# Kernel optimization log

Measured on AMD Instinct MI355X. Metric: run time of the kernel, lower is better.

## Reference

```python
import jax, jax.numpy as jnp
import numpy as np


def setup_inputs() -> dict:
    key = jax.random.key(0)
    k1, k2, k3, k4 = jax.random.split(key, 4)
    B, N, d_in, d_out = 8, 2048, 256, 256
    x = jax.random.normal(k1, (B, N, d_in), dtype=jnp.float32)
    adj_hat = jax.random.uniform(k2, (B, N, N), dtype=jnp.float32)
    W = jax.random.normal(k3, (d_out, d_in), dtype=jnp.float32) * (1.0 / np.sqrt(d_in))
    b = jax.random.normal(k4, (d_out,), dtype=jnp.float32) * 0.01
    return {"x": x, "adj_hat": adj_hat, "W": W, "b": b}


def reference(x, adj_hat, W, b):
    # Degrees from adj = adj_hat - I (i.e. without self loops): row sum minus diagonal.
    N = adj_hat.shape[1]
    diag = jnp.diagonal(adj_hat, axis1=-2, axis2=-1)          # [B, N]
    d = adj_hat.sum(axis=-1) - diag                           # [B, N]
    d_inv_sqrt = jnp.power(d, -0.5)                           # [B, N]
    # dad = D^-1/2 @ adj_hat @ D^-1/2  ==  d_i * a_ij * d_j (elementwise broadcast)
    dad = d_inv_sqrt[:, :, None] * adj_hat * d_inv_sqrt[:, None, :]  # [B, N, N]
    h = jnp.einsum('bnd,od->bno', x, W) + b                   # projection [B, N, d_out]
    return jnp.einsum('bnm,bmo->bno', dad, h)                 # [B, N, d_out]
```

## Files before the change

### kernel.cpp

```cpp
#include <hip/hip_runtime.h>
#include <hip/hip_bf16.h>


#define BATCH 8
#define NN    2048
#define DIN   256
#define DOUT  256
#define RTOT  (BATCH * NN)
#define AP    (NN + 32)
#define HP    (RTOT + 32)

typedef short  bf16x8  __attribute__((ext_vector_type(8)));
typedef short  short4v __attribute__((ext_vector_type(4)));
typedef float  f32x4   __attribute__((ext_vector_type(4)));

__device__ __forceinline__ short f2bf(float f) {
    union { float f; unsigned u; } v; v.f = f;
    unsigned r = v.u + 0x7fffu + ((v.u >> 16) & 1u);
    return (short)(r >> 16);
}

__device__ __forceinline__ void gl_lds16(const unsigned short* g, unsigned short* l) {
    __builtin_amdgcn_global_load_lds(
        (const __attribute__((address_space(1))) unsigned int*)g,
        (__attribute__((address_space(3))) unsigned int*)l, 16, 0, 0);
}

__global__ __launch_bounds__(256) void k_degree_cvt(const float* __restrict__ adj,
                                                    float* __restrict__ dis,
                                                    unsigned short* __restrict__ abf) {
    const int row = blockIdx.x;
    const int n = row & (NN - 1);
    const int tid = threadIdx.x;
    const float4* rp4 = (const float4*)(adj + (size_t)row * NN);
    unsigned short* op = abf + (size_t)row * AP;

    float s = 0.f;
#pragma unroll
    for (int i = 0; i < 2; i++) {
        float4 v = rp4[tid + i * 256];
        s += (v.x + v.y) + (v.z + v.w);
        short4v sv = { f2bf(v.x), f2bf(v.y), f2bf(v.z), f2bf(v.w) };
        *(short4v*)(op + 4 * (tid + i * 256)) = sv;
    }
#pragma unroll
    for (int off = 32; off; off >>= 1) s += __shfl_down(s, off);
    __shared__ float red[4];
    if ((tid & 63) == 0) red[tid >> 6] = s;
    __syncthreads();
    if (tid == 0) {
        float tot  = (red[0] + red[1]) + (red[2] + red[3]);
        float diag = ((const float*)rp4)[n];
        dis[row]   = rsqrtf(tot - diag);
    }
}

__global__ __launch_bounds__(256) void k_proj(const float* __restrict__ x,
                                              const float* __restrict__ W,
                                              const float* __restrict__ bias,
                                              const float* __restrict__ dis,
                                              unsigned short* __restrict__ hT) {
    const int mt  = blockIdx.y;
    const int nt  = blockIdx.x;
    const int tid = threadIdx.x;
    const int w = tid >> 6, lane = tid & 63;
    const int wr = w >> 1, wc = w & 1;
    const int l16 = lane & 15, quad = lane >> 4;

    __shared__ short As[128][32];
    __shared__ short Bs[128][32];

    f32x4 acc[4][4];
#pragma unroll
    for (int i = 0; i < 4; i++)
#pragma unroll
        for (int j = 0; j < 4; j++) acc[i][j] = (f32x4){0.f, 0.f, 0.f, 0.f};

    const float4* Wf4 = (const float4*)(W + (size_t)mt * 128 * DIN);
    const float4* Xf4 = (const float4*)(x + (size_t)nt * 128 * DIN);

    for (int kk = 0; kk < DIN / 32; kk++) {
        const int k0 = kk * 32;
        __syncthreads();
#pragma unroll
        for (int it = 0; it < 4; it++) {
            int idx = tid + it * 256;
            int r = idx >> 3, c = idx & 7;
            float4 va = Wf4[(size_t)r * (DIN / 4) + (k0 >> 2) + c];
            float4 vb = Xf4[(size_t)r * (DIN / 4) + (k0 >> 2) + c];
            short4v sa = { f2bf(va.x), f2bf(va.y), f2bf(va.z), f2bf(va.w) };
            short4v sb = { f2bf(vb.x), f2bf(vb.y), f2bf(vb.z), f2bf(vb.w) };
            *(short4v*)&As[r][c * 4] = sa;
            *(short4v*)&Bs[r][c * 4] = sb;
        }
        __syncthreads();
        bf16x8 af[4], bfv[4];
#pragma unroll
        for (int i = 0; i < 4; i++) af[i]  = *(bf16x8*)&As[wr * 64 + i * 16 + l16][quad * 8];
#pragma unroll
        for (int j = 0; j < 4; j++) bfv[j] = *(bf16x8*)&Bs[wc * 64 + j * 16 + l16][quad * 8];
#pragma unroll
        for (int i = 0; i < 4; i++)
#pragma unroll
            for (int j = 0; j < 4; j++)
                acc[i][j] = __builtin_amdgcn_mfma_f32_16x16x32_bf16(af[i], bfv[j], acc[i][j], 0, 0, 0);
    }

#pragma unroll
    for (int i = 0; i < 4; i++) {
        const int orow_base = mt * 128 + wr * 64 + i * 16 + quad * 4;
#pragma unroll
        for (int r = 0; r < 4; r++) {
            const int orow = orow_base + r;
            const float bb = bias[orow];
#pragma unroll
            for (int j = 0; j < 4; j++) {
                const int col = nt * 128 + wc * 64 + j * 16 + l16;
                float v = (acc[i][j][r] + bb) * dis[col];
                hT[(size_t)orow * HP + col] = (unsigned short)f2bf(v);
            }
        }
    }
}

__global__ __launch_bounds__(256, 2) void k_main(const unsigned short* __restrict__ abf,
                                                 const unsigned short* __restrict__ hT,
                                                 const float* __restrict__ dis,
                                                 float* __restrict__ out) {
    const int bx    = blockIdx.x;
    const int b     = bx & 7;
    const int mtile = (bx >> 3) & 31;
    const int ctile = bx >> 8;
    const int n0    = mtile * 64;
    const int tid  = threadIdx.x;
    const int w    = tid >> 6, lane = tid & 63;
    const int l16  = lane & 15, quad = lane >> 4;
    const int lr   = lane >> 2;
    const int lc   = (lane & 3) * 8;

    __shared__ short As[2][64][32];
    __shared__ short Bs[2][128][32];

    const unsigned short* agp = abf + (size_t)(b * NN + n0 + w * 16 + lr) * AP + lc;
    const unsigned short* bgp0 = hT + (size_t)(ctile * 128 + w * 32 + lr) * HP + b * NN + lc;
    const unsigned short* bgp1 = bgp0 + (size_t)16 * HP;
    unsigned short* alp[2] = { (unsigned short*)&As[0][w * 16][0], (unsigned short*)&As[1][w * 16][0] };
    unsigned short* blp0[2] = { (unsigned short*)&Bs[0][w * 32][0], (unsigned short*)&Bs[1][w * 32][0] };
    unsigned short* blp1[2] = { (unsigned short*)&Bs[0][w * 32 + 16][0], (unsigned short*)&Bs[1][w * 32 + 16][0] };

    f32x4 acc[4][2];
#pragma unroll
    for (int i = 0; i < 4; i++)
#pragma unroll
        for (int j = 0; j < 2; j++) acc[i][j] = (f32x4){0.f, 0.f, 0.f, 0.f};

    gl_lds16(agp, alp[0]);
    gl_lds16(bgp0, blp0[0]);
    gl_lds16(bgp1, blp1[0]);

    for (int kk = 0; kk < NN / 32; kk++) {
        const int cur = kk & 1, nxt = cur ^ 1;
        __syncthreads();
        if (kk < NN / 32 - 1) {
            const int ko = (kk + 1) * 32;
            gl_lds16(agp + ko, alp[nxt]);
            gl_lds16(bgp0 + ko, blp0[nxt]);
            gl_lds16(bgp1 + ko, blp1[nxt]);
        }
        bf16x8 af[4], bfv[2];
#pragma unroll
        for (int i = 0; i < 4; i++) af[i]  = *(bf16x8*)&As[cur][i * 16 + l16][quad * 8];
#pragma unroll
        for (int j = 0; j < 2; j++) bfv[j] = *(bf16x8*)&Bs[cur][w * 32 + j * 16 + l16][quad * 8];
#pragma unroll
        for (int i = 0; i < 4; i++)
#pragma unroll
            for (int j = 0; j < 2; j++)
                acc[i][j] = __builtin_amdgcn_mfma_f32_16x16x32_bf16(af[i], bfv[j], acc[i][j], 0, 0, 0);
    }

    const float* disb = dis + (size_t)b * NN;
#pragma unroll
    for (int i = 0; i < 4; i++) {
#pragma unroll
        for (int r = 0; r < 4; r++) {
            const int nrow = n0 + i * 16 + quad * 4 + r;
            const float dn = disb[nrow];
#pragma unroll
            for (int j = 0; j < 2; j++) {
                const int ocol = ctile * 128 + w * 32 + j * 16 + l16;
                out[((size_t)b * NN + nrow) * DOUT + ocol] = dn * acc[i][j][r];
            }
        }
    }
}

extern "C" void kernel_launch(void* const* d_in, const int* in_sizes, int n_in,
                              void* d_out, int out_size, void* d_ws, size_t ws_size,
                              hipStream_t stream) {
    const float* x    = (const float*)d_in[0];
    const float* adj  = (const float*)d_in[1];
    const float* W    = (const float*)d_in[2];
    const float* bias = (const float*)d_in[3];
    float* out = (float*)d_out;

    float* dis = (float*)d_ws;
    unsigned short* hT  = (unsigned short*)((char*)d_ws + 65536);
    unsigned short* abf = (unsigned short*)((char*)d_ws + 65536 + (size_t)DOUT * HP * 2);

    k_degree_cvt<<<RTOT, 256, 0, stream>>>(adj, dis, abf);
    k_proj<<<dim3(128, 2), 256, 0, stream>>>(x, W, bias, dis, hT);
    k_main<<<512, 256, 0, stream>>>(abf, hT, dis, out);
}
```

Baseline: 263.0 us.

## Deepen main GEMM LDS prefetch to four-slot pipeline with explicit vmcnt waits

```diff
diff --git a/kernel.cpp b/kernel.cpp
--- a/kernel.cpp
+++ b/kernel.cpp
@@ -138,15 +138,12 @@
     const int lr   = lane >> 2;
     const int lc   = (lane & 3) * 8;
 
-    __shared__ short As[2][64][32];
-    __shared__ short Bs[2][128][32];
-
-    const unsigned short* agp = abf + (size_t)(b * NN + n0 + w * 16 + lr) * AP + lc;
+    __shared__ short As[4][64][32];
+    __shared__ short Bs[4][128][32];
+
+    const unsigned short* agp  = abf + (size_t)(b * NN + n0 + w * 16 + lr) * AP + lc;
     const unsigned short* bgp0 = hT + (size_t)(ctile * 128 + w * 32 + lr) * HP + b * NN + lc;
     const unsigned short* bgp1 = bgp0 + (size_t)16 * HP;
-    unsigned short* alp[2] = { (unsigned short*)&As[0][w * 16][0], (unsigned short*)&As[1][w * 16][0] };
-    unsigned short* blp0[2] = { (unsigned short*)&Bs[0][w * 32][0], (unsigned short*)&Bs[1][w * 32][0] };
-    unsigned short* blp1[2] = { (unsigned short*)&Bs[0][w * 32 + 16][0], (unsigned short*)&Bs[1][w * 32 + 16][0] };
 
     f32x4 acc[4][2];
 #pragma unroll
@@ -154,30 +151,49 @@
 #pragma unroll
         for (int j = 0; j < 2; j++) acc[i][j] = (f32x4){0.f, 0.f, 0.f, 0.f};
 
-    gl_lds16(agp, alp[0]);
-    gl_lds16(bgp0, blp0[0]);
-    gl_lds16(bgp1, blp1[0]);
-
-    for (int kk = 0; kk < NN / 32; kk++) {
-        const int cur = kk & 1, nxt = cur ^ 1;
-        __syncthreads();
-        if (kk < NN / 32 - 1) {
-            const int ko = (kk + 1) * 32;
-            gl_lds16(agp + ko, alp[nxt]);
-            gl_lds16(bgp0 + ko, blp0[nxt]);
-            gl_lds16(bgp1 + ko, blp1[nxt]);
-        }
-        bf16x8 af[4], bfv[2];
-#pragma unroll
-        for (int i = 0; i < 4; i++) af[i]  = *(bf16x8*)&As[cur][i * 16 + l16][quad * 8];
-#pragma unroll
-        for (int j = 0; j < 2; j++) bfv[j] = *(bf16x8*)&Bs[cur][w * 32 + j * 16 + l16][quad * 8];
-#pragma unroll
-        for (int i = 0; i < 4; i++)
-#pragma unroll
-            for (int j = 0; j < 2; j++)
-                acc[i][j] = __builtin_amdgcn_mfma_f32_16x16x32_bf16(af[i], bfv[j], acc[i][j], 0, 0, 0);
-    }
+#define STAGE(slot, kw) do {                                            \
+        const int _ko = (kw) * 32;                                      \
+        gl_lds16(agp + _ko,  (unsigned short*)&As[slot][w * 16][0]);    \
+        gl_lds16(bgp0 + _ko, (unsigned short*)&Bs[slot][w * 32][0]);    \
+        gl_lds16(bgp1 + _ko, (unsigned short*)&Bs[slot][w * 32 + 16][0]); \
+    } while (0)
+
+#define CONSUME(slot) do {                                              \
+        bf16x8 af[4], bfv[2];                                           \
+        _Pragma("unroll")                                               \
+        for (int _i = 0; _i < 4; _i++)                                  \
+            af[_i]  = *(bf16x8*)&As[slot][_i * 16 + l16][quad * 8];     \
+        _Pragma("unroll")                                               \
+        for (int _j = 0; _j < 2; _j++)                                  \
+            bfv[_j] = *(bf16x8*)&Bs[slot][w * 32 + _j * 16 + l16][quad * 8]; \
+        _Pragma("unroll")                                               \
+        for (int _i = 0; _i < 4; _i++)                                  \
+            _Pragma("unroll")                                           \
+            for (int _j = 0; _j < 2; _j++)                              \
+                acc[_i][_j] = __builtin_amdgcn_mfma_f32_16x16x32_bf16(  \
+                    af[_i], bfv[_j], acc[_i][_j], 0, 0, 0);             \
+    } while (0)
+
+    STAGE(0, 0);
+    STAGE(1, 1);
+    STAGE(2, 2);
+
+    for (int k = 0; k < 62; k++) {
+        asm volatile("s_waitcnt vmcnt(6)" ::: "memory");
+        asm volatile("s_barrier" ::: "memory");
+        if (k < 61) STAGE((k + 3) & 3, k + 3);
+        const int s = k & 3;
+        CONSUME(s);
+    }
+    asm volatile("s_waitcnt vmcnt(3)" ::: "memory");
+    asm volatile("s_barrier" ::: "memory");
+    CONSUME(2);
+    asm volatile("s_waitcnt vmcnt(0)" ::: "memory");
+    asm volatile("s_barrier" ::: "memory");
+    CONSUME(3);
+
+#undef STAGE
+#undef CONSUME
 
     const float* disb = dis + (size_t)b * NN;
 #pragma unroll
```

After: 270.0 us. +2.7%, slower.
